# Kernel tuning notes

Hardware: AMD Instinct MI355X
Metric: run time of the kernel (lower is better)

Reference implementation:

```python
import jax, jax.numpy as jnp
import numpy as np

NEG_SLOPE = 0.01  # torch nn.LeakyReLU default
N_NODES, N_EDGES, N_BATCH, L_PATH = 100000, 300000, 50000, 4
D_EMB, D_HID, N_HEADS = 128, 64, 8


def setup_inputs() -> dict:
    key = jax.random.key(0)
    ks = jax.random.split(key, 10)
    return {
        "batch_nodes": jax.random.randint(ks[0], (N_BATCH,), 0, N_NODES),
        "metapath_indices": jax.random.randint(ks[1], (N_EDGES, L_PATH), 0, N_NODES),
        "edge_dst": jax.random.randint(ks[2], (N_EDGES,), 0, N_NODES),
        "transformed_feature": jax.random.normal(ks[3], (N_NODES, D_EMB), jnp.float32),
        "W_i": jax.random.normal(ks[4], (D_HID, D_EMB), jnp.float32) * 0.05,
        "W_p": jax.random.normal(ks[5], (D_HID, D_EMB), jnp.float32) * 0.05,
        "attn": jax.random.normal(ks[6], (1, N_HEADS, D_HID), jnp.float32) * 0.05,
        "W_th": jax.random.normal(ks[7], (N_HEADS, N_HEADS), jnp.float32) * 0.3,
        "W_gate": jax.random.normal(ks[8], (1, D_HID), jnp.float32) * 0.1,
        "b_gate": jnp.zeros((1,), jnp.float32),
    }


def reference(batch_nodes, metapath_indices, edge_dst, transformed_feature,
              W_i, W_p, attn, W_th, W_gate, b_gate):
    N = transformed_feature.shape[0]
    # node_type_specific_agg for mtype==1: h_src/h_dst through linear_i, h_p1/h_p2 through linear_p
    membd = transformed_feature[metapath_indices]                      # [E, 4, D_emb]
    edata = (membd[:, 0] + membd[:, 3]) @ W_i.T \
          + (membd[:, 1] + membd[:, 2]) @ W_p.T                        # [E, D]
    E, D = edata.shape
    H = attn.shape[1]
    # cat([edata]*H, dim=1).view(-1, H, D) duplicates edata per head
    efeat = jnp.broadcast_to(edata[:, None, :], (E, H, D))             # [E, H, D]
    # talking-heads attention logits, leaky-relu
    logits = (efeat * attn).sum(-1) @ W_th.T                           # [E, H]
    logits = jax.nn.leaky_relu(logits, NEG_SLOPE)
    # dgl edge_softmax: per-dst-node, per-head softmax over incoming edges (stable)
    m = jax.ops.segment_max(logits, edge_dst, num_segments=N)          # [N, H]
    ex = jnp.exp(logits - m[edge_dst])                                 # [E, H]
    den = jax.ops.segment_sum(ex, edge_dst, num_segments=N)            # [N, H]
    a = ex / den[edge_dst]                                             # [E, H]  (dropout rate 0)
    # message passing: ft = efeature * a, summed per dst node
    msgs = (efeat * a[:, :, None]).reshape(E, H * D)
    node_ft = jax.ops.segment_sum(msgs, edge_dst, num_segments=N)      # [N, H*D]
    result = node_ft[batch_nodes].reshape(-1, H, D)                    # [B, H, D]
    # gated multi-head attention: gate = mean over batch of fc_gate(result)
    gate = jnp.mean(result @ W_gate.T + b_gate, axis=0)                # [H, 1]
    result = result * gate[None]                                       # [B, H, D]
    return result.reshape(-1, H * D)
```

## Files before the change

### kernel.cpp

```cpp
#include <hip/hip_runtime.h>
#include <cstdint>
#include <cstddef>


typedef __attribute__((ext_vector_type(8))) short bf16x8;
typedef __attribute__((ext_vector_type(4))) float f32x4;

__device__ __forceinline__ unsigned short f2bf(float f) {
    unsigned u = __float_as_uint(f);
    unsigned r = u + 0x7fffu + ((u >> 16) & 1u);
    return (unsigned short)(r >> 16);
}
__device__ __forceinline__ float bf2f(unsigned short h) {
    return __uint_as_float((unsigned)h << 16);
}

__global__ __launch_bounds__(256) void k_prepW(
    const float* __restrict__ Wi, const float* __restrict__ Wp,
    unsigned short* __restrict__ Whi, unsigned short* __restrict__ Wlo) {
    int t = blockIdx.x * 256 + threadIdx.x;
    if (t >= 16384) return;
    int j = t & 7, L = (t >> 3) & 63, c = (t >> 9) & 7, s = t >> 12;
    int k = s * 32 + (L >> 4) * 8 + j;
    int n = c * 16 + (L & 15);
    float v = (n < 64) ? Wi[n * 128 + k] : Wp[(n - 64) * 128 + k];
    unsigned short h = f2bf(v);
    Whi[t] = h;
    Wlo[t] = f2bf(v - bf2f(h));
}

__global__ __launch_bounds__(256) void k_dense(
    const float* __restrict__ feat, const unsigned short* __restrict__ Whi,
    const unsigned short* __restrict__ Wlo, unsigned short* __restrict__ Ybf, int M) {
    int wave = threadIdx.x >> 6;
    int L = threadIdx.x & 63;
    int m = L & 15, q = L >> 4;
    int R0 = blockIdx.x * 64 + wave * 16;

    f32x4 acc[8];
#pragma unroll
    for (int c = 0; c < 8; ++c) acc[c] = (f32x4){0.f, 0.f, 0.f, 0.f};

    int rowc = R0 + m; if (rowc > M - 1) rowc = M - 1;
    const float* arow = feat + (size_t)rowc * 128;

    for (int s = 0; s < 4; ++s) {
        const float4* ap = (const float4*)(arow + s * 32 + q * 8);
        float4 a0 = ap[0], a1 = ap[1];
        float av[8] = {a0.x, a0.y, a0.z, a0.w, a1.x, a1.y, a1.z, a1.w};
        bf16x8 ahi, alo;
#pragma unroll
        for (int j = 0; j < 8; ++j) {
            unsigned short h = f2bf(av[j]);
            ahi[j] = (short)h;
            alo[j] = (short)f2bf(av[j] - bf2f(h));
        }
#pragma unroll
        for (int c = 0; c < 8; ++c) {
            const bf16x8 bh = *(const bf16x8*)(Whi + ((s * 8 + c) * 512 + L * 8));
            const bf16x8 bl = *(const bf16x8*)(Wlo + ((s * 8 + c) * 512 + L * 8));
            acc[c] = __builtin_amdgcn_mfma_f32_16x16x32_bf16(ahi, bh, acc[c], 0, 0, 0);
            acc[c] = __builtin_amdgcn_mfma_f32_16x16x32_bf16(ahi, bl, acc[c], 0, 0, 0);
            acc[c] = __builtin_amdgcn_mfma_f32_16x16x32_bf16(alo, bh, acc[c], 0, 0, 0);
        }
    }
#pragma unroll
    for (int c = 0; c < 8; ++c) {
#pragma unroll
        for (int r = 0; r < 4; ++r) {
            int row = R0 + q * 4 + r;
            if (row < M) Ybf[(size_t)row * 128 + c * 16 + m] = f2bf(acc[c][r]);
        }
    }
}

__global__ __launch_bounds__(256) void k_P(
    const unsigned short* __restrict__ Ybf, const float* __restrict__ attn,
    float* __restrict__ P, int N) {
    int n = blockIdx.x * 4 + (threadIdx.x >> 6);
    int lane = threadIdx.x & 63;
    if (n >= N) return;
    const unsigned short* yr = Ybf + (size_t)n * 128;
    float y0 = bf2f(yr[2 * lane]), y1 = bf2f(yr[2 * lane + 1]);
    int d0 = (2 * lane) & 63, d1 = (2 * lane + 1) & 63;
#pragma unroll
    for (int i = 0; i < 8; ++i) {
        float p = y0 * attn[i * 64 + d0] + y1 * attn[i * 64 + d1];
#pragma unroll
        for (int o = 1; o < 32; o <<= 1) p += __shfl_xor(p, o);
        if (lane == 0)  P[n * 16 + i] = p;
        if (lane == 32) P[n * 16 + 8 + i] = p;
    }
}

__global__ __launch_bounds__(256) void k_count(
    const int* __restrict__ batch_nodes, int* __restrict__ mult, int B) {
    int i = blockIdx.x * 256 + threadIdx.x;
    if (i < B) atomicAdd(&mult[batch_nodes[i]], 1);
}

__global__ __launch_bounds__(256) void k_hist(
    const int* __restrict__ edge_dst, const int* __restrict__ mult,
    int* __restrict__ count, int E) {
    int e = blockIdx.x * 256 + threadIdx.x;
    if (e >= E) return;
    int d = edge_dst[e];
    if (mult[d] > 0) atomicAdd(&count[d], 1);
}

__global__ __launch_bounds__(256) void k_scan1(
    const int* __restrict__ count, int* __restrict__ excl, int* __restrict__ partials, int N) {
    __shared__ int lds[256];
    int t = threadIdx.x, i = blockIdx.x * 256 + t;
    int c = (i < N) ? count[i] : 0;
    lds[t] = c; __syncthreads();
    for (int o = 1; o < 256; o <<= 1) {
        int v = (t >= o) ? lds[t - o] : 0;
        __syncthreads(); lds[t] += v; __syncthreads();
    }
    if (i < N) excl[i] = lds[t] - c;
    if (t == 255) partials[blockIdx.x] = lds[255];
}
__global__ __launch_bounds__(512) void k_scan2(
    const int* __restrict__ partials, int* __restrict__ blockoff,
    int* __restrict__ offsets, int nb, int N) {
    __shared__ int lds[512];
    int t = threadIdx.x;
    int c = (t < nb) ? partials[t] : 0;
    lds[t] = c; __syncthreads();
    for (int o = 1; o < 512; o <<= 1) {
        int v = (t >= o) ? lds[t - o] : 0;
        __syncthreads(); lds[t] += v; __syncthreads();
    }
    if (t < nb) blockoff[t] = lds[t] - c;
    if (t == nb - 1) offsets[N] = lds[t];
}
__global__ __launch_bounds__(256) void k_scan3(
    const int* __restrict__ excl, const int* __restrict__ blockoff,
    int* __restrict__ offsets, int* __restrict__ cursor, int N) {
    int i = blockIdx.x * 256 + threadIdx.x;
    if (i < N) {
        int o = excl[i] + blockoff[i >> 8];
        offsets[i] = o; cursor[i] = o;
    }
}

__global__ __launch_bounds__(256) void k_scatter(
    const int* __restrict__ edge_dst, const int* __restrict__ mult,
    int* __restrict__ cursor, int* __restrict__ csr, int E) {
    int e = blockIdx.x * 256 + threadIdx.x;
    if (e >= E) return;
    int d = edge_dst[e];
    if (mult[d] > 0) {
        int pos = atomicAdd(&cursor[d], 1);
        csr[pos] = e;
    }
}

__global__ __launch_bounds__(256) void k_logits(
    const int* __restrict__ csr, const int* __restrict__ pEc,
    const int* __restrict__ mp, const float* __restrict__ P,
    const float* __restrict__ Wth, float* __restrict__ logits,
    int4* __restrict__ mpc) {
    int Ec = *pEc;
    int i = blockIdx.x * 32 + (threadIdx.x >> 3);
    if (i >= Ec) return;
    int h = threadIdx.x & 7;
    int e = csr[i];
    int4 rows = *(const int4*)(mp + (size_t)e * 4);
    float s = P[rows.x * 16 + h] + P[rows.w * 16 + h]
            + P[rows.y * 16 + 8 + h] + P[rows.z * 16 + 8 + h];
    int gbase = threadIdx.x & ~7;
    float l = 0.f;
#pragma unroll
    for (int j = 0; j < 8; ++j) {
        float sj = __shfl(s, gbase + j);
        l += Wth[h * 8 + j] * sj;
    }
    l = l > 0.f ? l : 0.01f * l;
    logits[(size_t)i * 8 + h] = l;
    if (h == 0) mpc[i] = rows;
}

__global__ __launch_bounds__(256) void k_node_agg(
    const unsigned short* __restrict__ Ybf, const float* __restrict__ logits,
    const int4* __restrict__ mpc, const int* __restrict__ offsets,
    const int* __restrict__ mult, const float* __restrict__ Wg,
    unsigned short* __restrict__ nftb, float* __restrict__ gate_part, int N) {
    int n = blockIdx.x * 4 + (threadIdx.x >> 6);
    int lane = threadIdx.x & 63;
    if (n >= N) return;
    int m = mult[n];
    if (m == 0) return;
    int beg = offsets[n], end = offsets[n + 1];

    float mx[8];
#pragma unroll
    for (int h = 0; h < 8; ++h) mx[h] = -1e30f;
    for (int j = beg; j < end; ++j) {
        const float4* lp = (const float4*)(logits + (size_t)j * 8);
        float4 l0 = lp[0], l1 = lp[1];
        mx[0] = fmaxf(mx[0], l0.x); mx[1] = fmaxf(mx[1], l0.y);
        mx[2] = fmaxf(mx[2], l0.z); mx[3] = fmaxf(mx[3], l0.w);
        mx[4] = fmaxf(mx[4], l1.x); mx[5] = fmaxf(mx[5], l1.y);
        mx[6] = fmaxf(mx[6], l1.z); mx[7] = fmaxf(mx[7], l1.w);
    }
    float den[8], acc[8];
#pragma unroll
    for (int h = 0; h < 8; ++h) { den[h] = 0.f; acc[h] = 0.f; }
    for (int j = beg; j < end; ++j) {
        const float4* lp = (const float4*)(logits + (size_t)j * 8);
        float4 l0 = lp[0], l1 = lp[1];
        int4 rows = mpc[j];
        float ed = bf2f(Ybf[(size_t)rows.x * 128 + lane])
                 + bf2f(Ybf[(size_t)rows.w * 128 + lane])
                 + bf2f(Ybf[(size_t)rows.y * 128 + 64 + lane])
                 + bf2f(Ybf[(size_t)rows.z * 128 + 64 + lane]);
        float w0 = __expf(l0.x - mx[0]), w1 = __expf(l0.y - mx[1]);
        float w2 = __expf(l0.z - mx[2]), w3 = __expf(l0.w - mx[3]);
        float w4 = __expf(l1.x - mx[4]), w5 = __expf(l1.y - mx[5]);
        float w6 = __expf(l1.z - mx[6]), w7 = __expf(l1.w - mx[7]);
        den[0] += w0; den[1] += w1; den[2] += w2; den[3] += w3;
        den[4] += w4; den[5] += w5; den[6] += w6; den[7] += w7;
        acc[0] += w0 * ed; acc[1] += w1 * ed; acc[2] += w2 * ed; acc[3] += w3 * ed;
        acc[4] += w4 * ed; acc[5] += w5 * ed; acc[6] += w6 * ed; acc[7] += w7 * ed;
    }
#pragma unroll
    for (int h = 0; h < 8; ++h) {
        float r = (end > beg) ? 1.f / den[h] : 0.f;
        acc[h] *= r;
    }

    unsigned short* base = nftb + (size_t)n * 512;
#pragma unroll
    for (int h = 0; h < 8; ++h) base[h * 64 + lane] = f2bf(acc[h]);

    float wg = Wg[lane];
    float myg = 0.f;
#pragma unroll
    for (int h = 0; h < 8; ++h) {
        float p = acc[h] * wg;
#pragma unroll
        for (int o = 32; o > 0; o >>= 1) p += __shfl_xor(p, o);
        if (lane == h) myg = p;
    }
    if (lane < 8)
        atomicAdd(&gate_part[(blockIdx.x & 1023) * 8 + lane], (float)m * myg);
}

__global__ __launch_bounds__(256) void k_gatefinal(
    const float* __restrict__ gate_part, const float* __restrict__ b_gate,
    float* __restrict__ gate, int B) {
    __shared__ float lds[256];
    int t = threadIdx.x;
    int h = t & 7, g = t >> 3;
    float s = 0.f;
    for (int b = g; b < 1024; b += 32) s += gate_part[b * 8 + h];
    lds[t] = s; __syncthreads();
    if (t < 8) {
        float tot = 0.f;
        for (int gg = 0; gg < 32; ++gg) tot += lds[gg * 8 + t];
        gate[t] = tot / (float)B + b_gate[0];
    }
}

__global__ __launch_bounds__(256) void k_output(
    const unsigned short* __restrict__ nftb, const int* __restrict__ batch_nodes,
    const float* __restrict__ gate, float* __restrict__ out, int B) {
    int idx = blockIdx.x * 256 + threadIdx.x;
    int total = B * 128;
    if (idx >= total) return;
    int b = idx >> 7;
    int rem4 = idx & 127;
    int h = rem4 >> 4;
    int n = batch_nodes[b];
    ushort4 v = *(const ushort4*)(nftb + (size_t)n * 512 + rem4 * 4);
    float g = gate[h];
    float4 o;
    o.x = bf2f(v.x) * g; o.y = bf2f(v.y) * g;
    o.z = bf2f(v.z) * g; o.w = bf2f(v.w) * g;
    *(float4*)(out + (size_t)idx * 4) = o;
}

extern "C" void kernel_launch(void* const* d_in, const int* in_sizes, int n_in,
                              void* d_out, int out_size, void* d_ws, size_t ws_size,
                              hipStream_t stream) {
    const int*   batch_nodes = (const int*)d_in[0];
    const int*   mp          = (const int*)d_in[1];
    const int*   edge_dst    = (const int*)d_in[2];
    const float* feat        = (const float*)d_in[3];
    const float* W_i         = (const float*)d_in[4];
    const float* W_p         = (const float*)d_in[5];
    const float* attn        = (const float*)d_in[6];
    const float* W_th        = (const float*)d_in[7];
    const float* W_gate      = (const float*)d_in[8];
    const float* b_gate      = (const float*)d_in[9];
    float* out = (float*)d_out;

    const int B = in_sizes[0];
    const int E = in_sizes[2];
    const int N = in_sizes[3] / 128;
    const int nb_scan = (N + 255) / 256;

    char* w = (char*)d_ws;
    auto alloc = [&](size_t bytes) -> void* {
        void* p = (void*)w;
        w += (bytes + 255) & ~(size_t)255;
        return p;
    };
    unsigned short* Whi = (unsigned short*)alloc(16384 * 2);
    unsigned short* Wlo = (unsigned short*)alloc(16384 * 2);
    unsigned short* Ybf = (unsigned short*)alloc((size_t)N * 128 * 2);
    float* P            = (float*)alloc((size_t)N * 16 * 4);
    float* logits       = (float*)alloc((size_t)E * 8 * 4);
    int4*  mpc          = (int4*)alloc((size_t)E * 16);
    int*   mult         = (int*)alloc((size_t)N * 4);
    int*   count        = (int*)alloc((size_t)N * 4);
    int*   excl         = (int*)alloc((size_t)N * 4);
    int*   offsets      = (int*)alloc((size_t)(N + 1) * 4);
    int*   cursor       = (int*)alloc((size_t)N * 4);
    int*   partials     = (int*)alloc(512 * 4);
    int*   blockoff     = (int*)alloc(512 * 4);
    int*   csr          = (int*)alloc((size_t)E * 4);
    unsigned short* nftb = (unsigned short*)alloc((size_t)N * 512 * 2);
    float* gate_part    = (float*)alloc(1024 * 8 * 4);
    float* gate         = (float*)alloc(256);

    hipMemsetAsync(mult, 0, (size_t)N * 4, stream);
    hipMemsetAsync(count, 0, (size_t)N * 4, stream);
    hipMemsetAsync(gate_part, 0, 1024 * 8 * 4, stream);

    k_prepW<<<64, 256, 0, stream>>>(W_i, W_p, Whi, Wlo);
    k_dense<<<(N + 63) / 64, 256, 0, stream>>>(feat, Whi, Wlo, Ybf, N);
    k_P<<<(N + 3) / 4, 256, 0, stream>>>(Ybf, attn, P, N);

    k_count<<<(B + 255) / 256, 256, 0, stream>>>(batch_nodes, mult, B);
    k_hist<<<(E + 255) / 256, 256, 0, stream>>>(edge_dst, mult, count, E);
    k_scan1<<<nb_scan, 256, 0, stream>>>(count, excl, partials, N);
    k_scan2<<<1, 512, 0, stream>>>(partials, blockoff, offsets, nb_scan, N);
    k_scan3<<<nb_scan, 256, 0, stream>>>(excl, blockoff, offsets, cursor, N);
    k_scatter<<<(E + 255) / 256, 256, 0, stream>>>(edge_dst, mult, cursor, csr, E);

    const int* pEc = offsets + N;
    k_logits<<<(E + 31) / 32, 256, 0, stream>>>(csr, pEc, mp, P, W_th, logits, mpc);
    k_node_agg<<<(N + 3) / 4, 256, 0, stream>>>(Ybf, logits, mpc, offsets, mult,
                                                W_gate, nftb, gate_part, N);
    k_gatefinal<<<1, 256, 0, stream>>>(gate_part, b_gate, gate, B);
    k_output<<<(B * 128 + 255) / 256, 256, 0, stream>>>(nftb, batch_nodes, gate, out, B);
}
```

Before: 362.1 us.

## Fuse kernels: P into dense GEMM, scatter with logits, merged scans, online softmax

The edge-logit projection P is now computed inside the dense MFMA kernel from its accumulators, and weights are staged through LDS. The count kernel is folded into weight prep, and the memsets are merged into one. The scan2/scan3 pair becomes a single kernel that re-reduces the partials per block. Scatter and logits are fused, so logits are written straight to their CSR slot and the csr array is gone. Node aggregation switches to a one-pass online softmax, which saves a pass over logits but adds an extra exp per head per edge.

```diff
diff --git a/kernel.cpp b/kernel.cpp
--- a/kernel.cpp
+++ b/kernel.cpp
@@ -15,10 +15,12 @@
     return __uint_as_float((unsigned)h << 16);
 }
 
-__global__ __launch_bounds__(256) void k_prepW(
+__global__ __launch_bounds__(256) void k_prep(
     const float* __restrict__ Wi, const float* __restrict__ Wp,
-    unsigned short* __restrict__ Whi, unsigned short* __restrict__ Wlo) {
+    unsigned short* __restrict__ Whi, unsigned short* __restrict__ Wlo,
+    const int* __restrict__ batch_nodes, int* __restrict__ mult, int B) {
     int t = blockIdx.x * 256 + threadIdx.x;
+    if (t < B) atomicAdd(&mult[batch_nodes[t]], 1);
     if (t >= 16384) return;
     int j = t & 7, L = (t >> 3) & 63, c = (t >> 9) & 7, s = t >> 12;
     int k = s * 32 + (L >> 4) * 8 + j;
@@ -31,9 +33,13 @@
 
 __global__ __launch_bounds__(256) void k_dense(
     const float* __restrict__ feat, const unsigned short* __restrict__ Whi,
-    const unsigned short* __restrict__ Wlo, unsigned short* __restrict__ Ybf, int M) {
-    int wave = threadIdx.x >> 6;
-    int L = threadIdx.x & 63;
+    const unsigned short* __restrict__ Wlo, const float* __restrict__ attn,
+    unsigned short* __restrict__ Ybf, float* __restrict__ P, int M) {
+    __shared__ unsigned short sBh[4096];
+    __shared__ unsigned short sBl[4096];
+    int t = threadIdx.x;
+    int wave = t >> 6;
+    int L = t & 63;
     int m = L & 15, q = L >> 4;
     int R0 = blockIdx.x * 64 + wave * 16;
 
@@ -45,6 +51,17 @@
     const float* arow = feat + (size_t)rowc * 128;
 
     for (int s = 0; s < 4; ++s) {
+        __syncthreads();
+        {
+            bf16x8* shp = (bf16x8*)sBh;
+            bf16x8* slp = (bf16x8*)sBl;
+            const bf16x8* gh = (const bf16x8*)(Whi + s * 4096);
+            const bf16x8* gl = (const bf16x8*)(Wlo + s * 4096);
+            shp[t] = gh[t]; shp[t + 256] = gh[t + 256];
+            slp[t] = gl[t]; slp[t + 256] = gl[t + 256];
+        }
+        __syncthreads();
+
         const float4* ap = (const float4*)(arow + s * 32 + q * 8);
         float4 a0 = ap[0], a1 = ap[1];
         float av[8] = {a0.x, a0.y, a0.z, a0.w, a1.x, a1.y, a1.z, a1.w};
@@ -57,8 +74,8 @@
         }
 #pragma unroll
         for (int c = 0; c < 8; ++c) {
-            const bf16x8 bh = *(const bf16x8*)(Whi + ((s * 8 + c) * 512 + L * 8));
-            const bf16x8 bl = *(const bf16x8*)(Wlo + ((s * 8 + c) * 512 + L * 8));
+            const bf16x8 bh = *(const bf16x8*)(sBh + c * 512 + L * 8);
+            const bf16x8 bl = *(const bf16x8*)(sBl + c * 512 + L * 8);
             acc[c] = __builtin_amdgcn_mfma_f32_16x16x32_bf16(ahi, bh, acc[c], 0, 0, 0);
             acc[c] = __builtin_amdgcn_mfma_f32_16x16x32_bf16(ahi, bl, acc[c], 0, 0, 0);
             acc[c] = __builtin_amdgcn_mfma_f32_16x16x32_bf16(alo, bh, acc[c], 0, 0, 0);
@@ -72,31 +89,28 @@
             if (row < M) Ybf[(size_t)row * 128 + c * 16 + m] = f2bf(acc[c][r]);
         }
     }
-}
-
-__global__ __launch_bounds__(256) void k_P(
-    const unsigned short* __restrict__ Ybf, const float* __restrict__ attn,
-    float* __restrict__ P, int N) {
-    int n = blockIdx.x * 4 + (threadIdx.x >> 6);
-    int lane = threadIdx.x & 63;
-    if (n >= N) return;
-    const unsigned short* yr = Ybf + (size_t)n * 128;
-    float y0 = bf2f(yr[2 * lane]), y1 = bf2f(yr[2 * lane + 1]);
-    int d0 = (2 * lane) & 63, d1 = (2 * lane + 1) & 63;
 #pragma unroll
     for (int i = 0; i < 8; ++i) {
-        float p = y0 * attn[i * 64 + d0] + y1 * attn[i * 64 + d1];
-#pragma unroll
-        for (int o = 1; o < 32; o <<= 1) p += __shfl_xor(p, o);
-        if (lane == 0)  P[n * 16 + i] = p;
-        if (lane == 32) P[n * 16 + 8 + i] = p;
-    }
-}
-
-__global__ __launch_bounds__(256) void k_count(
-    const int* __restrict__ batch_nodes, int* __restrict__ mult, int B) {
-    int i = blockIdx.x * 256 + threadIdx.x;
-    if (i < B) atomicAdd(&mult[batch_nodes[i]], 1);
+        float a0 = attn[i * 64 + m];
+        float a1 = attn[i * 64 + 16 + m];
+        float a2 = attn[i * 64 + 32 + m];
+        float a3 = attn[i * 64 + 48 + m];
+#pragma unroll
+        for (int r = 0; r < 4; ++r) {
+            int row = R0 + q * 4 + r;
+            float pi = acc[0][r] * a0 + acc[1][r] * a1 + acc[2][r] * a2 + acc[3][r] * a3;
+            float pp = acc[4][r] * a0 + acc[5][r] * a1 + acc[6][r] * a2 + acc[7][r] * a3;
+#pragma unroll
+            for (int o = 1; o < 16; o <<= 1) {
+                pi += __shfl_xor(pi, o);
+                pp += __shfl_xor(pp, o);
+            }
+            if (row < M) {
+                if (m == i)     P[(size_t)row * 16 + i] = pi;
+                if (m == i + 8) P[(size_t)row * 16 + 8 + i] = pp;
+            }
+        }
+    }
 }
 
 __global__ __launch_bounds__(256) void k_hist(
@@ -121,56 +135,46 @@
     if (i < N) excl[i] = lds[t] - c;
     if (t == 255) partials[blockIdx.x] = lds[255];
 }
-__global__ __launch_bounds__(512) void k_scan2(
-    const int* __restrict__ partials, int* __restrict__ blockoff,
-    int* __restrict__ offsets, int nb, int N) {
-    __shared__ int lds[512];
-    int t = threadIdx.x;
-    int c = (t < nb) ? partials[t] : 0;
-    lds[t] = c; __syncthreads();
-    for (int o = 1; o < 512; o <<= 1) {
-        int v = (t >= o) ? lds[t - o] : 0;
-        __syncthreads(); lds[t] += v; __syncthreads();
-    }
-    if (t < nb) blockoff[t] = lds[t] - c;
-    if (t == nb - 1) offsets[N] = lds[t];
-}
-__global__ __launch_bounds__(256) void k_scan3(
-    const int* __restrict__ excl, const int* __restrict__ blockoff,
+
+__global__ __launch_bounds__(256) void k_scan23(
+    const int* __restrict__ excl, const int* __restrict__ partials,
     int* __restrict__ offsets, int* __restrict__ cursor, int N) {
-    int i = blockIdx.x * 256 + threadIdx.x;
+    __shared__ int sacc[256];
+    int bid = blockIdx.x, t = threadIdx.x;
+    int s = 0;
+    for (int j = t; j < bid; j += 256) s += partials[j];
+    sacc[t] = s; __syncthreads();
+#pragma unroll
+    for (int o = 128; o > 0; o >>= 1) {
+        if (t < o) sacc[t] += sacc[t + o];
+        __syncthreads();
+    }
+    int boff = sacc[0];
+    int i = bid * 256 + t;
     if (i < N) {
-        int o = excl[i] + blockoff[i >> 8];
+        int o = excl[i] + boff;
         offsets[i] = o; cursor[i] = o;
     }
-}
-
-__global__ __launch_bounds__(256) void k_scatter(
+    if (t == 0 && bid == gridDim.x - 1) offsets[N] = boff + partials[bid];
+}
+
+__global__ __launch_bounds__(256) void k_scatter_logits(
     const int* __restrict__ edge_dst, const int* __restrict__ mult,
-    int* __restrict__ cursor, int* __restrict__ csr, int E) {
-    int e = blockIdx.x * 256 + threadIdx.x;
+    int* __restrict__ cursor, const int* __restrict__ mp,
+    const float* __restrict__ P, const float* __restrict__ Wth,
+    float* __restrict__ logits, int4* __restrict__ mpc, int E) {
+    int e = blockIdx.x * 32 + (threadIdx.x >> 3);
     if (e >= E) return;
+    int h = threadIdx.x & 7;
     int d = edge_dst[e];
-    if (mult[d] > 0) {
-        int pos = atomicAdd(&cursor[d], 1);
-        csr[pos] = e;
-    }
-}
-
-__global__ __launch_bounds__(256) void k_logits(
-    const int* __restrict__ csr, const int* __restrict__ pEc,
-    const int* __restrict__ mp, const float* __restrict__ P,
-    const float* __restrict__ Wth, float* __restrict__ logits,
-    int4* __restrict__ mpc) {
-    int Ec = *pEc;
-    int i = blockIdx.x * 32 + (threadIdx.x >> 3);
-    if (i >= Ec) return;
-    int h = threadIdx.x & 7;
-    int e = csr[i];
+    if (mult[d] == 0) return;
+    int pos = 0;
+    if (h == 0) pos = atomicAdd(&cursor[d], 1);
+    int gbase = threadIdx.x & ~7;
+    pos = __shfl(pos, gbase);
     int4 rows = *(const int4*)(mp + (size_t)e * 4);
-    float s = P[rows.x * 16 + h] + P[rows.w * 16 + h]
-            + P[rows.y * 16 + 8 + h] + P[rows.z * 16 + 8 + h];
-    int gbase = threadIdx.x & ~7;
+    float s = P[(size_t)rows.x * 16 + h] + P[(size_t)rows.w * 16 + h]
+            + P[(size_t)rows.y * 16 + 8 + h] + P[(size_t)rows.z * 16 + 8 + h];
     float l = 0.f;
 #pragma unroll
     for (int j = 0; j < 8; ++j) {
@@ -178,8 +182,8 @@
         l += Wth[h * 8 + j] * sj;
     }
     l = l > 0.f ? l : 0.01f * l;
-    logits[(size_t)i * 8 + h] = l;
-    if (h == 0) mpc[i] = rows;
+    logits[(size_t)pos * 8 + h] = l;
+    if (h == 0) mpc[pos] = rows;
 }
 
 __global__ __launch_bounds__(256) void k_node_agg(
@@ -194,20 +198,10 @@
     if (m == 0) return;
     int beg = offsets[n], end = offsets[n + 1];
 
-    float mx[8];
-#pragma unroll
-    for (int h = 0; h < 8; ++h) mx[h] = -1e30f;
-    for (int j = beg; j < end; ++j) {
-        const float4* lp = (const float4*)(logits + (size_t)j * 8);
-        float4 l0 = lp[0], l1 = lp[1];
-        mx[0] = fmaxf(mx[0], l0.x); mx[1] = fmaxf(mx[1], l0.y);
-        mx[2] = fmaxf(mx[2], l0.z); mx[3] = fmaxf(mx[3], l0.w);
-        mx[4] = fmaxf(mx[4], l1.x); mx[5] = fmaxf(mx[5], l1.y);
-        mx[6] = fmaxf(mx[6], l1.z); mx[7] = fmaxf(mx[7], l1.w);
-    }
-    float den[8], acc[8];
-#pragma unroll
-    for (int h = 0; h < 8; ++h) { den[h] = 0.f; acc[h] = 0.f; }
+    float mx[8], den[8], acc[8];
+#pragma unroll
+    for (int h = 0; h < 8; ++h) { mx[h] = -1e30f; den[h] = 0.f; acc[h] = 0.f; }
+
     for (int j = beg; j < end; ++j) {
         const float4* lp = (const float4*)(logits + (size_t)j * 8);
         float4 l0 = lp[0], l1 = lp[1];
@@ -216,14 +210,18 @@
                  + bf2f(Ybf[(size_t)rows.w * 128 + lane])
                  + bf2f(Ybf[(size_t)rows.y * 128 + 64 + lane])
                  + bf2f(Ybf[(size_t)rows.z * 128 + 64 + lane]);
-        float w0 = __expf(l0.x - mx[0]), w1 = __expf(l0.y - mx[1]);
-        float w2 = __expf(l0.z - mx[2]), w3 = __expf(l0.w - mx[3]);
-        float w4 = __expf(l1.x - mx[4]), w5 = __expf(l1.y - mx[5]);
-        float w6 = __expf(l1.z - mx[6]), w7 = __expf(l1.w - mx[7]);
-        den[0] += w0; den[1] += w1; den[2] += w2; den[3] += w3;
-        den[4] += w4; den[5] += w5; den[6] += w6; den[7] += w7;
-        acc[0] += w0 * ed; acc[1] += w1 * ed; acc[2] += w2 * ed; acc[3] += w3 * ed;
-        acc[4] += w4 * ed; acc[5] += w5 * ed; acc[6] += w6 * ed; acc[7] += w7 * ed;
+#define OSM_STEP(H, LV)                                            \
+        {                                                          \
+            float nm = fmaxf(mx[H], (LV));                         \
+            float cr = __expf(mx[H] - nm);                         \
+            float w  = __expf((LV) - nm);                          \
+            den[H] = den[H] * cr + w;                              \
+            acc[H] = acc[H] * cr + w * ed;                         \
+            mx[H] = nm;                                            \
+        }
+        OSM_STEP(0, l0.x) OSM_STEP(1, l0.y) OSM_STEP(2, l0.z) OSM_STEP(3, l0.w)
+        OSM_STEP(4, l1.x) OSM_STEP(5, l1.y) OSM_STEP(6, l1.z) OSM_STEP(7, l1.w)
+#undef OSM_STEP
     }
 #pragma unroll
     for (int h = 0; h < 8; ++h) {
@@ -314,35 +312,29 @@
     float* P            = (float*)alloc((size_t)N * 16 * 4);
     float* logits       = (float*)alloc((size_t)E * 8 * 4);
     int4*  mpc          = (int4*)alloc((size_t)E * 16);
-    int*   mult         = (int*)alloc((size_t)N * 4);
-    int*   count        = (int*)alloc((size_t)N * 4);
+    size_t zero_bytes   = (size_t)N * 4 + (size_t)N * 4 + 1024 * 8 * 4;
+    int*   mult         = (int*)alloc(zero_bytes);
+    int*   count        = mult + N;
+    float* gate_part    = (float*)(count + N);
     int*   excl         = (int*)alloc((size_t)N * 4);
     int*   offsets      = (int*)alloc((size_t)(N + 1) * 4);
     int*   cursor       = (int*)alloc((size_t)N * 4);
     int*   partials     = (int*)alloc(512 * 4);
-    int*   blockoff     = (int*)alloc(512 * 4);
-    int*   csr          = (int*)alloc((size_t)E * 4);
     unsigned short* nftb = (unsigned short*)alloc((size_t)N * 512 * 2);
-    float* gate_part    = (float*)alloc(1024 * 8 * 4);
     float* gate         = (float*)alloc(256);
 
-    hipMemsetAsync(mult, 0, (size_t)N * 4, stream);
-    hipMemsetAsync(count, 0, (size_t)N * 4, stream);
-    hipMemsetAsync(gate_part, 0, 1024 * 8 * 4, stream);
-
-    k_prepW<<<64, 256, 0, stream>>>(W_i, W_p, Whi, Wlo);
-    k_dense<<<(N + 63) / 64, 256, 0, stream>>>(feat, Whi, Wlo, Ybf, N);
-    k_P<<<(N + 3) / 4, 256, 0, stream>>>(Ybf, attn, P, N);
-
-    k_count<<<(B + 255) / 256, 256, 0, stream>>>(batch_nodes, mult, B);
+    hipMemsetAsync(mult, 0, zero_bytes, stream);
+
+    int prep_work = (B > 16384) ? B : 16384;
+    k_prep<<<(prep_work + 255) / 256, 256, 0, stream>>>(W_i, W_p, Whi, Wlo,
+                                                        batch_nodes, mult, B);
+    k_dense<<<(N + 63) / 64, 256, 0, stream>>>(feat, Whi, Wlo, attn, Ybf, P, N);
+
     k_hist<<<(E + 255) / 256, 256, 0, stream>>>(edge_dst, mult, count, E);
     k_scan1<<<nb_scan, 256, 0, stream>>>(count, excl, partials, N);
-    k_scan2<<<1, 512, 0, stream>>>(partials, blockoff, offsets, nb_scan, N);
-    k_scan3<<<nb_scan, 256, 0, stream>>>(excl, blockoff, offsets, cursor, N);
-    k_scatter<<<(E + 255) / 256, 256, 0, stream>>>(edge_dst, mult, cursor, csr, E);
-
-    const int* pEc = offsets + N;
-    k_logits<<<(E + 31) / 32, 256, 0, stream>>>(csr, pEc, mp, P, W_th, logits, mpc);
+    k_scan23<<<nb_scan, 256, 0, stream>>>(excl, partials, offsets, cursor, N);
+    k_scatter_logits<<<(E + 31) / 32, 256, 0, stream>>>(edge_dst, mult, cursor,
+                                                        mp, P, W_th, logits, mpc, E);
     k_node_agg<<<(N + 3) / 4, 256, 0, stream>>>(Ybf, logits, mpc, offsets, mult,
                                                 W_gate, nftb, gate_part, N);
     k_gatefinal<<<1, 256, 0, stream>>>(gate_part, b_gate, gate, B);
```

New measurement: 317.5 us. -12.3%, faster.
